# Performance work log

Measured on AMD Instinct MI355X. Metric: run time of the kernel, lower is better.

Reference implementation:

```python
import jax, jax.numpy as jnp
import numpy as np

N_HEADS = 4
NS_STEPS = 5
NS_EPS = 1e-7

def newtonschulz5(G):
    # G: [out, in]; quintic Newton-Schulz, 5 steps. out==in here so no transpose branch needed,
    # but keep the static-shape check for faithfulness.
    a, b, c = 3.4445, -4.775, 2.0315
    X = G / (jnp.linalg.norm(G) + NS_EPS)
    transposed = G.shape[0] > G.shape[1]
    if transposed:
        X = X.T
    def step(X, _):
        A = X @ X.T
        B = b * A + c * (A @ A)
        return a * X + B @ X, None
    X, _ = jax.lax.scan(step, X, None, length=NS_STEPS)
    if transposed:
        X = X.T
    return X

def setup_inputs() -> dict:
    key = jax.random.key(0)
    k1, k2, k3, k4, k5 = jax.random.split(key, 5)
    B, S, D_in, D_out, r = 4, 2048, 4096, 4096, 16
    init_std = 0.01 / np.sqrt(D_out * r)
    return {
        "x": jax.random.normal(k1, (B, S, D_in), dtype=jnp.float32),
        "W": jax.random.normal(k2, (D_out, D_in), dtype=jnp.float32) * 0.02,
        "bias": jax.random.normal(k3, (D_out,), dtype=jnp.float32) * 0.02,
        "lora_A": jax.random.normal(k4, (r, D_in), dtype=jnp.float32),
        "lora_B": jax.random.normal(k5, (D_out, r), dtype=jnp.float32) * init_std,
    }

def reference(x, W, bias, lora_A, lora_B):
    # base linear (frozen weights); dropout is identity (p=0 / eval)
    base_out = jnp.einsum('bsi,oi->bso', x, W) + bias
    r, D_in = lora_A.shape
    D_out = lora_B.shape[0]
    hr = r // N_HEADS
    Ah = lora_A.reshape(N_HEADS, hr, D_in)                       # [h, hr, in]
    Bh = lora_B.reshape(D_out, N_HEADS, hr).transpose(1, 0, 2)    # [h, out, hr]
    G = jnp.einsum('hor,hri->hoi', Bh, Ah)                        # [h, out, in]
    alpha = jnp.sqrt(jnp.sum(G * G, axis=(1, 2)))                 # per-head Frobenius norm
    M = jax.vmap(newtonschulz5)(G)                                # [h, out, in]
    lora_out = jnp.einsum('h,hoi,bsi->bso', alpha, M, x)
    return base_out + lora_out
```

## Files before the change

kernel.cpp:

```cpp
#include <hip/hip_runtime.h>
#include <math.h>

#define MDIM 8192
#define NDIM 4096
#define KDIM 4096

typedef __attribute__((ext_vector_type(8))) _Float16 h8;
typedef __attribute__((ext_vector_type(4))) _Float16 h4;
typedef __attribute__((ext_vector_type(4))) float f32x4;

typedef const __attribute__((address_space(1))) void* gas_ptr;
typedef __attribute__((address_space(3))) void* las_ptr;

__device__ inline void load16_to_lds(const void* g, void* l) {
  __builtin_amdgcn_global_load_lds((gas_ptr)g, (las_ptr)l, 16, 0, 0);
}

__device__ inline void mm4(const double* A, const double* B, double* C) {
#pragma unroll
  for (int p = 0; p < 4; ++p)
#pragma unroll
    for (int q = 0; q < 4; ++q) {
      double s = 0.0;
#pragma unroll
      for (int r = 0; r < 4; ++r) s += A[p * 4 + r] * B[r * 4 + q];
      C[p * 4 + q] = s;
    }
}
__device__ inline void mm4_bt(const double* A, const double* B, double* C) {
#pragma unroll
  for (int p = 0; p < 4; ++p)
#pragma unroll
    for (int q = 0; q < 4; ++q) {
      double s = 0.0;
#pragma unroll
      for (int r = 0; r < 4; ++r) s += A[p * 4 + r] * B[q * 4 + r];
      C[p * 4 + q] = s;
    }
}

__global__ void ns_kernel(const float* __restrict__ lora_A,
                          const float* __restrict__ lora_B,
                          float* __restrict__ E) {
  const int h = blockIdx.x;
  const int tid = threadIdx.x;
  const int lane = tid & 63;
  const int wave = tid >> 6;

  float gu[16], gv[16];
#pragma unroll
  for (int e = 0; e < 16; ++e) { gu[e] = 0.f; gv[e] = 0.f; }

  for (int o = tid; o < NDIM; o += 256) {
    const float4 bv = *(const float4*)(lora_B + (size_t)o * 16 + h * 4);
    const float bb[4] = {bv.x, bv.y, bv.z, bv.w};
#pragma unroll
    for (int p = 0; p < 4; ++p)
#pragma unroll
      for (int q = 0; q < 4; ++q) gu[p * 4 + q] += bb[p] * bb[q];
  }
  for (int i = tid; i < KDIM; i += 256) {
    float aa[4];
#pragma unroll
    for (int p = 0; p < 4; ++p) aa[p] = lora_A[(size_t)(h * 4 + p) * KDIM + i];
#pragma unroll
    for (int p = 0; p < 4; ++p)
#pragma unroll
      for (int q = 0; q < 4; ++q) gv[p * 4 + q] += aa[p] * aa[q];
  }

#pragma unroll
  for (int e = 0; e < 16; ++e) {
#pragma unroll
    for (int off = 32; off > 0; off >>= 1) {
      gu[e] += __shfl_down(gu[e], off, 64);
      gv[e] += __shfl_down(gv[e], off, 64);
    }
  }
  __shared__ float pu[4][16], pv[4][16];
  if (lane == 0) {
#pragma unroll
    for (int e = 0; e < 16; ++e) { pu[wave][e] = gu[e]; pv[wave][e] = gv[e]; }
  }
  __syncthreads();

  if (tid == 0) {
    double gud[16], gvd[16];
#pragma unroll
    for (int e = 0; e < 16; ++e) {
      gud[e] = (double)pu[0][e] + pu[1][e] + pu[2][e] + pu[3][e];
      gvd[e] = (double)pv[0][e] + pv[1][e] + pv[2][e] + pv[3][e];
    }
    double tr = 0.0;
#pragma unroll
    for (int e = 0; e < 16; ++e) tr += gud[e] * gvd[e];
    const double alpha = sqrt(tr);
    const double n0 = alpha + 1e-7;

    double C[16] = {0};
    C[0] = C[5] = C[10] = C[15] = 1.0 / n0;

    const double a = 3.4445, b = -4.775, c = 2.0315;
    for (int it = 0; it < 5; ++it) {
      double T1[16], D[16], DG[16], DGD[16], GuC[16], F[16], Cn[16];
      mm4(C, gvd, T1);
      mm4_bt(T1, C, D);
      mm4(D, gud, DG);
      mm4(DG, D, DGD);
      mm4(gud, C, GuC);
#pragma unroll
      for (int e = 0; e < 16; ++e) F[e] = b * D[e] + c * DGD[e];
      mm4(F, GuC, Cn);
#pragma unroll
      for (int e = 0; e < 16; ++e) C[e] = a * C[e] + Cn[e];
    }
#pragma unroll
    for (int e = 0; e < 16; ++e) E[h * 16 + e] = (float)(alpha * C[e]);
  }
}

__global__ void prep_kernel(const float* __restrict__ x,
                            const float* __restrict__ W,
                            const float* __restrict__ lora_A,
                            const float* __restrict__ lora_B,
                            const float* __restrict__ E,
                            _Float16* __restrict__ Wh,
                            _Float16* __restrict__ Xh) {
  const int tid = threadIdx.x;
  if (blockIdx.x < NDIM) {
    const int o = blockIdx.x;
    __shared__ float coef[16];
    if (tid < 16) {
      const int h = tid >> 2, q = tid & 3;
      float s = 0.f;
#pragma unroll
      for (int p = 0; p < 4; ++p)
        s += lora_B[(size_t)o * 16 + h * 4 + p] * E[h * 16 + p * 4 + q];
      coef[tid] = s;
    }
    __syncthreads();
    float cf[16];
#pragma unroll
    for (int k = 0; k < 16; ++k) cf[k] = coef[k];

    for (int i = tid * 4; i < KDIM; i += 1024) {
      float4 acc = *(const float4*)(W + (size_t)o * KDIM + i);
#pragma unroll
      for (int k = 0; k < 16; ++k) {
        const float4 av = *(const float4*)(lora_A + (size_t)k * KDIM + i);
        acc.x += cf[k] * av.x; acc.y += cf[k] * av.y;
        acc.z += cf[k] * av.z; acc.w += cf[k] * av.w;
      }
      h4 pk;
      pk[0] = (_Float16)acc.x; pk[1] = (_Float16)acc.y;
      pk[2] = (_Float16)acc.z; pk[3] = (_Float16)acc.w;
      *(h4*)(Wh + (size_t)o * KDIM + i) = pk;
    }
  } else {
    const size_t t = (size_t)(blockIdx.x - NDIM) * 256 + tid;
    const size_t base = t * 8;
    const float4 a = *(const float4*)(x + base);
    const float4 b = *(const float4*)(x + base + 4);
    h8 o;
    o[0] = (_Float16)a.x; o[1] = (_Float16)a.y; o[2] = (_Float16)a.z; o[3] = (_Float16)a.w;
    o[4] = (_Float16)b.x; o[5] = (_Float16)b.y; o[6] = (_Float16)b.z; o[7] = (_Float16)b.w;
    *(h8*)(Xh + base) = o;
  }
}

__launch_bounds__(512, 2)
__global__ void gemm_kernel(const _Float16* __restrict__ Xh,
                            const _Float16* __restrict__ Wh,
                            const float* __restrict__ bias,
                            float* __restrict__ out) {
  __shared__ __align__(16) _Float16 sA0h0[128 * 64], sA0h1[128 * 64];
  __shared__ __align__(16) _Float16 sA1h0[128 * 64], sA1h1[128 * 64];
  __shared__ __align__(16) _Float16 sB0h0[128 * 64], sB0h1[128 * 64];
  __shared__ __align__(16) _Float16 sB1h0[128 * 64], sB1h1[128 * 64];

  const int tid = threadIdx.x;
  const int lane = tid & 63;
  const int wave = tid >> 6;
  const int wm = wave >> 2;
  const int wn = wave & 3;
  const int quad = lane >> 4;
  const int r16 = lane & 15;
  const int sw = r16 & 7;

  const int lin = blockIdx.x;
  const int wg = (lin & 7) * 64 + (lin >> 3);
  const int bm = wg >> 4;
  const int bn = wg & 15;

  const int row0 = tid >> 3;
  const int lc0 = (tid & 7) ^ (row0 & 7);
  const size_t off0 = (size_t)row0 * KDIM + lc0 * 8;
  const int ldsb = tid * 16;
  const _Float16* pA0 = Xh + (size_t)(bm * 256) * KDIM;
  const _Float16* pA1 = pA0 + (size_t)128 * KDIM;
  const _Float16* pB0 = Wh + (size_t)(bn * 256) * KDIM;
  const _Float16* pB1 = pB0 + (size_t)128 * KDIM;

  const int aRow = (wm * 64 + r16) * 64;
  const int bRow = (wn * 32 + r16) * 64;
  const int c0 = (quad ^ sw) * 8;
  const int c1 = ((quad + 4) ^ sw) * 8;

  f32x4 acc[2][2][4][2] = {};

#define STAGE(arr, p, koff) do {                                               \
    load16_to_lds((p) + off0 + (koff), (char*)(arr) + ldsb);                   \
    load16_to_lds((p) + off0 + (size_t)64 * KDIM + (koff),                     \
                  (char*)(arr) + ldsb + 8192);                                 \
  } while (0)

#define FENCE() asm volatile("" ::: "memory")
#define BAR() do { FENCE(); __builtin_amdgcn_s_barrier(); FENCE(); } while (0)
#define VM4() asm volatile("s_waitcnt vmcnt(4)" ::: "memory")
#define VM0() asm volatile("s_waitcnt vmcnt(0)" ::: "memory")

#define PHASE(Aarr, Barr, mq, nq, STMT, WCNT) do {                             \
    h8 av[4][2], bv[2][2];                                                     \
    _Pragma("unroll")                                                          \
    for (int f = 0; f < 4; ++f) {                                              \
      av[f][0] = *(const h8*)&Aarr[aRow + f * 1024 + c0];                      \
      av[f][1] = *(const h8*)&Aarr[aRow + f * 1024 + c1];                      \
    }                                                                          \
    _Pragma("unroll")                                                          \
    for (int g = 0; g < 2; ++g) {                                              \
      bv[g][0] = *(const h8*)&Barr[bRow + g * 1024 + c0];                      \
      bv[g][1] = *(const h8*)&Barr[bRow + g * 1024 + c1];                      \
    }                                                                          \
    STMT;                                                                      \
    BAR();                                                                     \
    __builtin_amdgcn_s_setprio(1);                                             \
    _Pragma("unroll")                                                          \
    for (int f = 0; f < 4; ++f)                                                \
      _Pragma("unroll")                                                        \
      for (int g = 0; g < 2; ++g) {                                            \
        acc[mq][nq][f][g] = __builtin_amdgcn_mfma_f32_16x16x32_f16(            \
            av[f][0], bv[g][0], acc[mq][nq][f][g], 0, 0, 0);                   \
        acc[mq][nq][f][g] = __builtin_amdgcn_mfma_f32_16x16x32_f16(            \
            av[f][1], bv[g][1], acc[mq][nq][f][g], 0, 0, 0);                   \
      }                                                                        \
    __builtin_amdgcn_s_setprio(0);                                             \
    WCNT;                                                                      \
    BAR();                                                                     \
  } while (0)

#define TILE(t, cA0, cA1, cB0, cB1, oA1, oB1) do {                             \
    PHASE(cA0, cB0, 0, 0,                                                      \
          { if ((t) + 1 < NT) STAGE(oA1, pA1, ((t) + 1) * 64); }, ;);          \
    PHASE(cA0, cB1, 0, 1,                                                      \
          { if ((t) + 1 < NT) STAGE(oB1, pB1, ((t) + 1) * 64); }, ;);          \
    PHASE(cA1, cB0, 1, 0,                                                      \
          { if ((t) + 2 < NT) STAGE(cA0, pA0, ((t) + 2) * 64); }, ;);          \
    PHASE(cA1, cB1, 1, 1,                                                      \
          { if ((t) + 2 < NT) STAGE(cB0, pB0, ((t) + 2) * 64); },              \
          { if ((t) + 2 < NT) VM4(); else VM0(); });                           \
  } while (0)

  constexpr int NT = KDIM / 64;

  STAGE(sA0h0, pA0, 0);  STAGE(sB0h0, pB0, 0);
  STAGE(sA0h1, pA1, 0);  STAGE(sB0h1, pB1, 0);
  STAGE(sA1h0, pA0, 64); STAGE(sB1h0, pB0, 64);
  VM4();
  BAR();

#pragma unroll 1
  for (int t2 = 0; t2 < NT; t2 += 2) {
    TILE(t2,     sA0h0, sA0h1, sB0h0, sB0h1, sA1h1, sB1h1);
    TILE(t2 + 1, sA1h0, sA1h1, sB1h0, sB1h1, sA0h1, sB0h1);
  }

#pragma unroll
  for (int mq = 0; mq < 2; ++mq)
#pragma unroll
    for (int f = 0; f < 4; ++f) {
      float* po = out + (size_t)(bm * 256 + mq * 128 + wm * 64 + f * 16 + quad * 4) * NDIM;
#pragma unroll
      for (int nq = 0; nq < 2; ++nq)
#pragma unroll
        for (int g = 0; g < 2; ++g) {
          const int ocol = bn * 256 + nq * 128 + wn * 32 + g * 16 + r16;
          const float bb = bias[ocol];
          const f32x4 v = acc[mq][nq][f][g];
#pragma unroll
          for (int rg = 0; rg < 4; ++rg)
            po[(size_t)rg * NDIM + ocol] = v[rg] + bb;
        }
    }
}

extern "C" void kernel_launch(void* const* d_in, const int* in_sizes, int n_in,
                              void* d_out, int out_size, void* d_ws, size_t ws_size,
                              hipStream_t stream) {
  const float* x      = (const float*)d_in[0];
  const float* W      = (const float*)d_in[1];
  const float* bias   = (const float*)d_in[2];
  const float* lora_A = (const float*)d_in[3];
  const float* lora_B = (const float*)d_in[4];
  float* out = (float*)d_out;

  char* ws = (char*)d_ws;
  float* E = (float*)ws;
  _Float16* Wh = (_Float16*)(ws + 1024);
  _Float16* Xh = (_Float16*)(ws + 1024 + (size_t)NDIM * KDIM * 2);

  ns_kernel<<<dim3(4), dim3(256), 0, stream>>>(lora_A, lora_B, E);
  prep_kernel<<<dim3(NDIM + (MDIM * KDIM) / (256 * 8)), dim3(256), 0, stream>>>(
      x, W, lora_A, lora_B, E, Wh, Xh);
  gemm_kernel<<<dim3(512), dim3(512), 0, stream>>>(Xh, Wh, bias, out);
}
```

Before: 604.5 us.

## Restructure GEMM pipeline to reuse fragments and batch LoRA weight fold rows

The W-fold part of prep_kernel now handles 16 output rows per block. It stages a 1024-column chunk of lora_A in shared memory so the rank-16 A data is read once per 16 rows instead of once per row. The GEMM main loop switches from a 3-deep ring over half-tiles to a 2-buffer ping-pong over whole K tiles. Each phase prefetches the next tile's quarter, and the phases are ordered (00, 01, 11, 10) so the A or B register fragments carry over between adjacent phases and fewer LDS reads are needed. The cost is one less tile of prefetch depth, an explicit last-tile epilogue, and more live registers for the fragments.

Measured after the change: 602.9 us. No clear change (-0.3%).

```diff
diff --git a/kernel.cpp b/kernel.cpp
--- a/kernel.cpp
+++ b/kernel.cpp
@@ -127,37 +127,49 @@
                             _Float16* __restrict__ Wh,
                             _Float16* __restrict__ Xh) {
   const int tid = threadIdx.x;
-  if (blockIdx.x < NDIM) {
-    const int o = blockIdx.x;
-    __shared__ float coef[16];
-    if (tid < 16) {
-      const int h = tid >> 2, q = tid & 3;
+  if (blockIdx.x < 256) {
+    __shared__ float cf[16][16];
+    __shared__ __align__(16) float Asm[16][1024];
+    const int o0 = blockIdx.x * 16;
+    {
+      const int r = tid >> 4, kk = tid & 15, h = kk >> 2, q = kk & 3;
       float s = 0.f;
 #pragma unroll
       for (int p = 0; p < 4; ++p)
-        s += lora_B[(size_t)o * 16 + h * 4 + p] * E[h * 16 + p * 4 + q];
-      coef[tid] = s;
-    }
-    __syncthreads();
-    float cf[16];
-#pragma unroll
-    for (int k = 0; k < 16; ++k) cf[k] = coef[k];
-
-    for (int i = tid * 4; i < KDIM; i += 1024) {
-      float4 acc = *(const float4*)(W + (size_t)o * KDIM + i);
-#pragma unroll
-      for (int k = 0; k < 16; ++k) {
-        const float4 av = *(const float4*)(lora_A + (size_t)k * KDIM + i);
-        acc.x += cf[k] * av.x; acc.y += cf[k] * av.y;
-        acc.z += cf[k] * av.z; acc.w += cf[k] * av.w;
+        s += lora_B[(size_t)(o0 + r) * 16 + h * 4 + p] * E[h * 16 + p * 4 + q];
+      cf[r][kk] = s;
+    }
+    for (int kb = 0; kb < KDIM; kb += 1024) {
+      __syncthreads();
+#pragma unroll
+      for (int j = 0; j < 16; ++j) {
+        const int f4 = tid + j * 256;
+        const int k = f4 >> 8, c4 = f4 & 255;
+        *(float4*)&Asm[k][c4 * 4] =
+            *(const float4*)&lora_A[(size_t)k * KDIM + kb + (size_t)c4 * 4];
       }
-      h4 pk;
-      pk[0] = (_Float16)acc.x; pk[1] = (_Float16)acc.y;
-      pk[2] = (_Float16)acc.z; pk[3] = (_Float16)acc.w;
-      *(h4*)(Wh + (size_t)o * KDIM + i) = pk;
+      __syncthreads();
+      float4 av[16];
+#pragma unroll
+      for (int k = 0; k < 16; ++k) av[k] = *(const float4*)&Asm[k][tid * 4];
+#pragma unroll
+      for (int r = 0; r < 16; ++r) {
+        const size_t base = (size_t)(o0 + r) * KDIM + kb + tid * 4;
+        float4 acc = *(const float4*)&W[base];
+#pragma unroll
+        for (int k = 0; k < 16; ++k) {
+          const float cfv = cf[r][k];
+          acc.x += cfv * av[k].x; acc.y += cfv * av[k].y;
+          acc.z += cfv * av[k].z; acc.w += cfv * av[k].w;
+        }
+        h4 pk;
+        pk[0] = (_Float16)acc.x; pk[1] = (_Float16)acc.y;
+        pk[2] = (_Float16)acc.z; pk[3] = (_Float16)acc.w;
+        *(h4*)(Wh + base) = pk;
+      }
     }
   } else {
-    const size_t t = (size_t)(blockIdx.x - NDIM) * 256 + tid;
+    const size_t t = (size_t)(blockIdx.x - 256) * 256 + tid;
     const size_t base = t * 8;
     const float4 a = *(const float4*)(x + base);
     const float4 b = *(const float4*)(x + base + 4);
@@ -173,10 +185,10 @@
                             const _Float16* __restrict__ Wh,
                             const float* __restrict__ bias,
                             float* __restrict__ out) {
-  __shared__ __align__(16) _Float16 sA0h0[128 * 64], sA0h1[128 * 64];
-  __shared__ __align__(16) _Float16 sA1h0[128 * 64], sA1h1[128 * 64];
-  __shared__ __align__(16) _Float16 sB0h0[128 * 64], sB0h1[128 * 64];
-  __shared__ __align__(16) _Float16 sB1h0[128 * 64], sB1h1[128 * 64];
+  __shared__ __align__(16) _Float16 sA0_0[128 * 64], sA0_1[128 * 64];
+  __shared__ __align__(16) _Float16 sA1_0[128 * 64], sA1_1[128 * 64];
+  __shared__ __align__(16) _Float16 sB0_0[128 * 64], sB0_1[128 * 64];
+  __shared__ __align__(16) _Float16 sB1_0[128 * 64], sB1_1[128 * 64];
 
   const int tid = threadIdx.x;
   const int lane = tid & 63;
@@ -207,6 +219,7 @@
   const int c1 = ((quad + 4) ^ sw) * 8;
 
   f32x4 acc[2][2][4][2] = {};
+  h8 a0[4][2], a1[4][2], b0[2][2], b1[2][2];
 
 #define STAGE(arr, p, koff) do {                                               \
     load16_to_lds((p) + off0 + (koff), (char*)(arr) + ldsb);                   \
@@ -217,62 +230,72 @@
 #define FENCE() asm volatile("" ::: "memory")
 #define BAR() do { FENCE(); __builtin_amdgcn_s_barrier(); FENCE(); } while (0)
 #define VM4() asm volatile("s_waitcnt vmcnt(4)" ::: "memory")
+#define VM2() asm volatile("s_waitcnt vmcnt(2)" ::: "memory")
 #define VM0() asm volatile("s_waitcnt vmcnt(0)" ::: "memory")
 
-#define PHASE(Aarr, Barr, mq, nq, STMT, WCNT) do {                             \
-    h8 av[4][2], bv[2][2];                                                     \
-    _Pragma("unroll")                                                          \
+#define RDA(dst, Aarr) do { _Pragma("unroll")                                  \
     for (int f = 0; f < 4; ++f) {                                              \
-      av[f][0] = *(const h8*)&Aarr[aRow + f * 1024 + c0];                      \
-      av[f][1] = *(const h8*)&Aarr[aRow + f * 1024 + c1];                      \
-    }                                                                          \
-    _Pragma("unroll")                                                          \
+      dst[f][0] = *(const h8*)&Aarr[aRow + f * 1024 + c0];                     \
+      dst[f][1] = *(const h8*)&Aarr[aRow + f * 1024 + c1];                     \
+    } } while (0)
+#define RDB(dst, Barr) do { _Pragma("unroll")                                  \
     for (int g = 0; g < 2; ++g) {                                              \
-      bv[g][0] = *(const h8*)&Barr[bRow + g * 1024 + c0];                      \
-      bv[g][1] = *(const h8*)&Barr[bRow + g * 1024 + c1];                      \
-    }                                                                          \
-    STMT;                                                                      \
-    BAR();                                                                     \
+      dst[g][0] = *(const h8*)&Barr[bRow + g * 1024 + c0];                     \
+      dst[g][1] = *(const h8*)&Barr[bRow + g * 1024 + c1];                     \
+    } } while (0)
+
+#define MFMA16(MQ, NQ, AV, BV) do {                                            \
     __builtin_amdgcn_s_setprio(1);                                             \
     _Pragma("unroll")                                                          \
     for (int f = 0; f < 4; ++f)                                                \
       _Pragma("unroll")                                                        \
       for (int g = 0; g < 2; ++g) {                                            \
-        acc[mq][nq][f][g] = __builtin_amdgcn_mfma_f32_16x16x32_f16(            \
-            av[f][0], bv[g][0], acc[mq][nq][f][g], 0, 0, 0);                   \
-        acc[mq][nq][f][g] = __builtin_amdgcn_mfma_f32_16x16x32_f16(            \
-            av[f][1], bv[g][1], acc[mq][nq][f][g], 0, 0, 0);                   \
+        acc[MQ][NQ][f][g] = __builtin_amdgcn_mfma_f32_16x16x32_f16(            \
+            AV[f][0], BV[g][0], acc[MQ][NQ][f][g], 0, 0, 0);                   \
+        acc[MQ][NQ][f][g] = __builtin_amdgcn_mfma_f32_16x16x32_f16(            \
+            AV[f][1], BV[g][1], acc[MQ][NQ][f][g], 0, 0, 0);                   \
       }                                                                        \
     __builtin_amdgcn_s_setprio(0);                                             \
-    WCNT;                                                                      \
-    BAR();                                                                     \
   } while (0)
 
-#define TILE(t, cA0, cA1, cB0, cB1, oA1, oB1) do {                             \
-    PHASE(cA0, cB0, 0, 0,                                                      \
-          { if ((t) + 1 < NT) STAGE(oA1, pA1, ((t) + 1) * 64); }, ;);          \
-    PHASE(cA0, cB1, 0, 1,                                                      \
-          { if ((t) + 1 < NT) STAGE(oB1, pB1, ((t) + 1) * 64); }, ;);          \
-    PHASE(cA1, cB0, 1, 0,                                                      \
-          { if ((t) + 2 < NT) STAGE(cA0, pA0, ((t) + 2) * 64); }, ;);          \
-    PHASE(cA1, cB1, 1, 1,                                                      \
-          { if ((t) + 2 < NT) STAGE(cB0, pB0, ((t) + 2) * 64); },              \
-          { if ((t) + 2 < NT) VM4(); else VM0(); });                           \
+#define TILE(t, cA0, cA1, cB0, cB1, nA0, nA1, nB0, nB1) do {                   \
+    RDA(a0, cA0); RDB(b0, cB0); STAGE(nA0, pA0, ((t) + 1) * 64);               \
+    BAR(); MFMA16(0, 0, a0, b0); VM4(); BAR();                                 \
+    RDB(b1, cB1);                STAGE(nB0, pB0, ((t) + 1) * 64);              \
+    BAR(); MFMA16(0, 1, a0, b1); VM4(); BAR();                                 \
+    RDA(a1, cA1);                STAGE(nB1, pB1, ((t) + 1) * 64);              \
+    BAR(); MFMA16(1, 1, a1, b1);        BAR();                                 \
+    RDB(b0, cB0);                STAGE(nA1, pA1, ((t) + 1) * 64);              \
+    BAR(); MFMA16(1, 0, a1, b0); VM4(); BAR();                                 \
   } while (0)
 
+#define TILE_LAST(cA0, cA1, cB0, cB1) do {                                     \
+    RDA(a0, cA0); RDB(b0, cB0);                                                \
+    BAR(); MFMA16(0, 0, a0, b0); VM2(); BAR();                                 \
+    RDB(b1, cB1);                                                              \
+    BAR(); MFMA16(0, 1, a0, b1); VM0(); BAR();                                 \
+    RDA(a1, cA1);                                                              \
+    BAR(); MFMA16(1, 1, a1, b1);        BAR();                                 \
+    RDB(b0, cB0);                                                              \
+    BAR(); MFMA16(1, 0, a1, b0);        BAR();                                 \
+  } while (0)
+
   constexpr int NT = KDIM / 64;
 
-  STAGE(sA0h0, pA0, 0);  STAGE(sB0h0, pB0, 0);
-  STAGE(sA0h1, pA1, 0);  STAGE(sB0h1, pB1, 0);
-  STAGE(sA1h0, pA0, 64); STAGE(sB1h0, pB0, 64);
+  STAGE(sA0_0, pA0, 0);
+  STAGE(sB0_0, pB0, 0);
+  STAGE(sB1_0, pB1, 0);
+  STAGE(sA1_0, pA1, 0);
   VM4();
   BAR();
 
 #pragma unroll 1
-  for (int t2 = 0; t2 < NT; t2 += 2) {
-    TILE(t2,     sA0h0, sA0h1, sB0h0, sB0h1, sA1h1, sB1h1);
-    TILE(t2 + 1, sA1h0, sA1h1, sB1h0, sB1h1, sA0h1, sB0h1);
-  }
+  for (int t2 = 0; t2 < NT - 2; t2 += 2) {
+    TILE(t2,     sA0_0, sA1_0, sB0_0, sB1_0, sA0_1, sA1_1, sB0_1, sB1_1);
+    TILE(t2 + 1, sA0_1, sA1_1, sB0_1, sB1_1, sA0_0, sA1_0, sB0_0, sB1_0);
+  }
+  TILE(NT - 2, sA0_0, sA1_0, sB0_0, sB1_0, sA0_1, sA1_1, sB0_1, sB1_1);
+  TILE_LAST(sA0_1, sA1_1, sB0_1, sB1_1);
 
 #pragma unroll
   for (int mq = 0; mq < 2; ++mq)
@@ -309,7 +332,7 @@
   _Float16* Xh = (_Float16*)(ws + 1024 + (size_t)NDIM * KDIM * 2);
 
   ns_kernel<<<dim3(4), dim3(256), 0, stream>>>(lora_A, lora_B, E);
-  prep_kernel<<<dim3(NDIM + (MDIM * KDIM) / (256 * 8)), dim3(256), 0, stream>>>(
+  prep_kernel<<<dim3(256 + (MDIM * KDIM) / (256 * 8)), dim3(256), 0, stream>>>(
       x, W, lora_A, lora_B, E, Wh, Xh);
   gemm_kernel<<<dim3(512), dim3(512), 0, stream>>>(Xh, Wh, bias, out);
 }
```
